# Kernel tuning notes

Hardware: AMD Instinct MI355X
Metric: run time of the kernel (lower is better)

## Reference

```python
import jax, jax.numpy as jnp
import numpy as np
import math

B, T, N_CTX, H = 4, 512, 2048, 1024
NUM_HEADS, NUM_INSTRUMENTS, MAX_BARS = 16, 16, 8
HEAD_DIM = H // NUM_HEADS


def setup_inputs() -> dict:
    key = jax.random.key(0)
    ks = jax.random.split(key, 16)
    s = 1.0 / math.sqrt(H)
    return {
        "query": jax.random.normal(ks[0], (B, T, H), jnp.float32),
        "context": jax.random.normal(ks[1], (B, N_CTX, H), jnp.float32),
        "instrument_ids": jax.random.randint(ks[2], (B, N_CTX), 0, NUM_INSTRUMENTS),
        "current_instrument_id": 3,
        "bar_offsets": jax.random.randint(ks[3], (B, N_CTX), 0, MAX_BARS),
        "Wq": jax.random.normal(ks[4], (H, H), jnp.float32) * s,
        "bq": jnp.zeros((H,), jnp.float32),
        "Wk": jax.random.normal(ks[5], (H, H), jnp.float32) * s,
        "bk": jnp.zeros((H,), jnp.float32),
        "Wv": jax.random.normal(ks[6], (H, H), jnp.float32) * s,
        "bv": jnp.zeros((H,), jnp.float32),
        "Wo": jax.random.normal(ks[7], (H, H), jnp.float32) * s,
        "bo": jnp.zeros((H,), jnp.float32),
        "inst_emb": jax.random.normal(ks[8], (NUM_INSTRUMENTS, H), jnp.float32),
        "bar_emb": jax.random.normal(ks[9], (MAX_BARS, H), jnp.float32),
    }


def reference(query, context, instrument_ids, current_instrument_id, bar_offsets,
              Wq, bq, Wk, bk, Wv, bv, Wo, bo, inst_emb, bar_emb):
    # current_instrument_id: python int -> broadcast to (B,)
    cur = jnp.full((B,), current_instrument_id, dtype=jnp.int64 if instrument_ids.dtype == jnp.int64 else jnp.int32)
    # add embeddings to query and context
    q = query + inst_emb[cur][:, None, :]                              # (B,T,H)
    ctx = context + inst_emb[instrument_ids] + bar_emb[jnp.clip(bar_offsets, 0, MAX_BARS - 1)]  # (B,N,H)
    # projections (torch Linear: x @ W.T + b)
    Q = (q @ Wq.T + bq).reshape(B, T, NUM_HEADS, HEAD_DIM).transpose(0, 2, 1, 3)      # (B,h,T,d)
    K = (ctx @ Wk.T + bk).reshape(B, N_CTX, NUM_HEADS, HEAD_DIM).transpose(0, 2, 1, 3)  # (B,h,N,d)
    V = (ctx @ Wv.T + bv).reshape(B, N_CTX, NUM_HEADS, HEAD_DIM).transpose(0, 2, 1, 3)  # (B,h,N,d)
    scores = jnp.einsum('bhtd,bhnd->bhtn', Q, K) / math.sqrt(HEAD_DIM)  # (B,h,T,N)
    # attend only to keys whose instrument differs from the current one
    keep = (instrument_ids != cur[:, None])[:, None, None, :]           # (B,1,1,N)
    scores = jnp.where(keep, scores, jnp.float32(-1e9))
    probs = jax.nn.softmax(scores, axis=-1)
    out = jnp.einsum('bhtn,bhnd->bhtd', probs, V).transpose(0, 2, 1, 3).reshape(B, T, H)
    return out @ Wo.T + bo
```

## Files before the change

kernel.cpp:

```cpp
#include <hip/hip_runtime.h>

#define H 1024
#define B_ 4
#define T_ 512
#define NCTX 2048
#define NH 16
#define HD 64

typedef __attribute__((ext_vector_type(8))) short bf16x8;
typedef __attribute__((ext_vector_type(4))) float f32x4;
typedef __attribute__((ext_vector_type(4))) short s16x4;

__device__ __forceinline__ ushort f2b(float f) {
  union { float f; unsigned u; } v; v.f = f;
  unsigned u = v.u;
  unsigned r = (u + 0x7FFFu + ((u >> 16) & 1u)) >> 16;
  return (ushort)r;
}

__device__ __forceinline__ unsigned cvt_pk_bf16(float lo, float hi) {
  unsigned r;
  asm("v_cvt_pk_bf16_f32 %0, %1, %2" : "=v"(r) : "v"(lo), "v"(hi));
  return r;
}

__device__ __forceinline__ void gld16(const void* g, void* l) {
  __builtin_amdgcn_global_load_lds((const __attribute__((address_space(1))) unsigned int*)g,
                                   (__attribute__((address_space(3))) unsigned int*)l, 16, 0, 0);
}


__global__ void prep_all(const float* __restrict__ query, const float* __restrict__ ctx,
                         const int* __restrict__ ids, const int* __restrict__ curp,
                         const int* __restrict__ bars,
                         const float* __restrict__ iemb, const float* __restrict__ bemb,
                         const float* __restrict__ Wq, const float* __restrict__ Wk,
                         const float* __restrict__ Wv, const float* __restrict__ Wo,
                         ushort* __restrict__ qin, ushort* __restrict__ ctxb,
                         ushort* __restrict__ Wqb, ushort* __restrict__ Wkb,
                         ushort* __restrict__ Wvb, ushort* __restrict__ Wob,
                         float* __restrict__ maskf) {
  int blk = blockIdx.x;
  if (blk < 8192) {
    int i = blk * 256 + threadIdx.x;
    int row = i >> 8;
    int c4 = i & 255;
    int id = ids[row];
    int bar = bars[row];
    bar = bar < 0 ? 0 : (bar > 7 ? 7 : bar);
    float4 v = ((const float4*)ctx)[i];
    float4 e = ((const float4*)(iemb + (size_t)id * H))[c4];
    float4 g = ((const float4*)(bemb + (size_t)bar * H))[c4];
    s16x4 o;
    o[0] = (short)f2b(v.x + e.x + g.x); o[1] = (short)f2b(v.y + e.y + g.y);
    o[2] = (short)f2b(v.z + e.z + g.z); o[3] = (short)f2b(v.w + e.w + g.w);
    ((s16x4*)ctxb)[i] = o;
  } else if (blk < 10240) {
    int cur = curp[0];
    int i = (blk - 8192) * 256 + threadIdx.x;
    int c4 = i & 255;
    float4 v = ((const float4*)query)[i];
    float4 e = ((const float4*)(iemb + (size_t)cur * H))[c4];
    s16x4 o;
    o[0] = (short)f2b(v.x + e.x); o[1] = (short)f2b(v.y + e.y);
    o[2] = (short)f2b(v.z + e.z); o[3] = (short)f2b(v.w + e.w);
    ((s16x4*)qin)[i] = o;
  } else if (blk < 14336) {
    int b2 = blk - 10240;
    int which = b2 >> 10;
    int i = (b2 & 1023) * 256 + threadIdx.x;
    const float* s = which == 0 ? Wq : which == 1 ? Wk : which == 2 ? Wv : Wo;
    ushort* d = which == 0 ? Wqb : which == 1 ? Wkb : which == 2 ? Wvb : Wob;
    float4 v = ((const float4*)s)[i];
    s16x4 o;
    o[0] = (short)f2b(v.x); o[1] = (short)f2b(v.y);
    o[2] = (short)f2b(v.z); o[3] = (short)f2b(v.w);
    ((s16x4*)d)[i] = o;
  } else {
    int cur = curp[0];
    int i = (blk - 14336) * 256 + threadIdx.x;
    maskf[i] = (ids[i] != cur) ? 0.f : -1e30f;
  }
}


__global__ __launch_bounds__(256) void proj_k(const ushort* __restrict__ Aq,
                                              const ushort* __restrict__ Actx,
                                              const ushort* __restrict__ WQ,
                                              const ushort* __restrict__ WK,
                                              const ushort* __restrict__ WV,
                                              const float* __restrict__ bQ,
                                              const float* __restrict__ bK,
                                              const float* __restrict__ bV,
                                              ushort* __restrict__ Qout,
                                              ushort* __restrict__ Kout,
                                              ushort* __restrict__ VTout) {
  const int id = blockIdx.x;
  const ushort* A;
  const ushort* W;
  const float* bias;
  int row0, col0, mode;
  ushort* Cout;
  if (id < 1024) {
    int xcd = id & 7, rest = id >> 3;
    int bx = rest & 15, by = (rest >> 4) * 8 + xcd;
    A = Actx; row0 = by * 128;
    if (bx < 8) { W = WK; bias = bK; col0 = bx * 128; mode = 0; Cout = Kout; }
    else        { W = WV; bias = bV; col0 = (bx - 8) * 128; mode = 1; Cout = VTout; }
  } else {
    int q = id - 1024;
    A = Aq; row0 = (q >> 3) * 128; col0 = (q & 7) * 128;
    W = WQ; bias = bQ; mode = 2; Cout = Qout;
  }

  __shared__ ushort As[2][128 * 32];
  __shared__ ushort Bs[2][128 * 32];
  const int tid = threadIdx.x;
  const int lane = tid & 63;
  const int wv = tid >> 6;
  const int wr = wv >> 1, wc = wv & 1;
  const int lo = lane & 15, hi = lane >> 4;

  f32x4 acc[4][4];
#pragma unroll
  for (int m = 0; m < 4; m++)
#pragma unroll
    for (int n = 0; n < 4; n++) acc[m][n] = (f32x4){0.f, 0.f, 0.f, 0.f};

#pragma unroll
  for (int c = 0; c < 2; c++) {
    int ia = wv * 128 + c * 64 + lane;
    int r = ia >> 2, s = ia & 3;
    int sg = s ^ (r & 3);
    gld16(A + (size_t)(row0 + r) * H + sg * 8, (char*)As[0] + (wv * 128 + c * 64) * 16);
    gld16(W + (size_t)(col0 + r) * H + sg * 8, (char*)Bs[0] + (wv * 128 + c * 64) * 16);
  }
  __syncthreads();

  int cur = 0;
  for (int kt = 0; kt < 32; kt++) {
    if (kt < 31) {
#pragma unroll
      for (int c = 0; c < 2; c++) {
        int ia = wv * 128 + c * 64 + lane;
        int r = ia >> 2, s = ia & 3;
        int sg = s ^ (r & 3);
        gld16(A + (size_t)(row0 + r) * H + (kt + 1) * 32 + sg * 8,
              (char*)As[cur ^ 1] + (wv * 128 + c * 64) * 16);
        gld16(W + (size_t)(col0 + r) * H + (kt + 1) * 32 + sg * 8,
              (char*)Bs[cur ^ 1] + (wv * 128 + c * 64) * 16);
      }
    }
    bf16x8 af[4], bfr[4];
#pragma unroll
    for (int m = 0; m < 4; m++) {
      int rr = wr * 64 + m * 16 + lo;
      af[m] = *(const bf16x8*)(As[cur] + rr * 32 + (hi ^ (rr & 3)) * 8);
    }
#pragma unroll
    for (int n = 0; n < 4; n++) {
      int rr = wc * 64 + n * 16 + lo;
      bfr[n] = *(const bf16x8*)(Bs[cur] + rr * 32 + (hi ^ (rr & 3)) * 8);
    }
#pragma unroll
    for (int m = 0; m < 4; m++)
#pragma unroll
      for (int n = 0; n < 4; n++)
        acc[m][n] = __builtin_amdgcn_mfma_f32_16x16x32_bf16(af[m], bfr[n], acc[m][n], 0, 0, 0);
    __syncthreads();
    cur ^= 1;
  }

#pragma unroll
  for (int m = 0; m < 4; m++) {
    int gr0 = row0 + wr * 64 + m * 16 + hi * 4;
#pragma unroll
    for (int n = 0; n < 4; n++) {
      int gc = col0 + wc * 64 + n * 16 + lo;
      float bv = bias[gc];
      if (mode == 0) {
#pragma unroll
        for (int r = 0; r < 4; r++)
          Cout[(size_t)(gr0 + r) * H + gc] = f2b(acc[m][n][r] + bv);
      } else if (mode == 1) {
        int bb = gr0 >> 11, n0 = gr0 & 2047;
        s16x4 o;
#pragma unroll
        for (int r = 0; r < 4; r++) o[r] = (short)f2b(acc[m][n][r] + bv);
        *(s16x4*)(Cout + (size_t)bb * (H * NCTX) + (size_t)gc * NCTX + n0) = o;
      } else {
#pragma unroll
        for (int r = 0; r < 4; r++)
          Cout[(size_t)(gr0 + r) * H + gc] = f2b((acc[m][n][r] + bv) * 0.125f);
      }
    }
  }
}


__global__ __launch_bounds__(256) void gemm_o(const ushort* __restrict__ A,
                                              const ushort* __restrict__ W,
                                              const float* __restrict__ bias,
                                              float* __restrict__ Cout) {
  __shared__ ushort As[2][128 * 32];
  __shared__ ushort Bs[2][128 * 32];
  const int tid = threadIdx.x;
  const int lane = tid & 63;
  const int wv = tid >> 6;
  const int wr = wv >> 1, wc = wv & 1;
  const int lo = lane & 15, hi = lane >> 4;
  const int row0 = blockIdx.y * 128, col0 = blockIdx.x * 128;

  f32x4 acc[4][4];
#pragma unroll
  for (int m = 0; m < 4; m++)
#pragma unroll
    for (int n = 0; n < 4; n++) acc[m][n] = (f32x4){0.f, 0.f, 0.f, 0.f};

#pragma unroll
  for (int c = 0; c < 2; c++) {
    int ia = wv * 128 + c * 64 + lane;
    int r = ia >> 2, s = ia & 3;
    int sg = s ^ (r & 3);
    gld16(A + (size_t)(row0 + r) * H + sg * 8, (char*)As[0] + (wv * 128 + c * 64) * 16);
    gld16(W + (size_t)(col0 + r) * H + sg * 8, (char*)Bs[0] + (wv * 128 + c * 64) * 16);
  }
  __syncthreads();

  int cur = 0;
  for (int kt = 0; kt < 32; kt++) {
    if (kt < 31) {
#pragma unroll
      for (int c = 0; c < 2; c++) {
        int ia = wv * 128 + c * 64 + lane;
        int r = ia >> 2, s = ia & 3;
        int sg = s ^ (r & 3);
        gld16(A + (size_t)(row0 + r) * H + (kt + 1) * 32 + sg * 8,
              (char*)As[cur ^ 1] + (wv * 128 + c * 64) * 16);
        gld16(W + (size_t)(col0 + r) * H + (kt + 1) * 32 + sg * 8,
              (char*)Bs[cur ^ 1] + (wv * 128 + c * 64) * 16);
      }
    }
    bf16x8 af[4], bfr[4];
#pragma unroll
    for (int m = 0; m < 4; m++) {
      int rr = wr * 64 + m * 16 + lo;
      af[m] = *(const bf16x8*)(As[cur] + rr * 32 + (hi ^ (rr & 3)) * 8);
    }
#pragma unroll
    for (int n = 0; n < 4; n++) {
      int rr = wc * 64 + n * 16 + lo;
      bfr[n] = *(const bf16x8*)(Bs[cur] + rr * 32 + (hi ^ (rr & 3)) * 8);
    }
#pragma unroll
    for (int m = 0; m < 4; m++)
#pragma unroll
      for (int n = 0; n < 4; n++)
        acc[m][n] = __builtin_amdgcn_mfma_f32_16x16x32_bf16(af[m], bfr[n], acc[m][n], 0, 0, 0);
    __syncthreads();
    cur ^= 1;
  }

#pragma unroll
  for (int m = 0; m < 4; m++) {
    int gr0 = row0 + wr * 64 + m * 16 + hi * 4;
#pragma unroll
    for (int n = 0; n < 4; n++) {
      int gc = col0 + wc * 64 + n * 16 + lo;
      float bv = bias[gc];
#pragma unroll
      for (int r = 0; r < 4; r++)
        Cout[(size_t)(gr0 + r) * H + gc] = acc[m][n][r] + bv;
    }
  }
}


#define NSPLIT 2
#define KVLEN (NCTX / NSPLIT)
#define NT_KV (KVLEN / 64)

__global__ __launch_bounds__(256) void attn_k(const ushort* __restrict__ Q,
                                              const ushort* __restrict__ K,
                                              const ushort* __restrict__ VT,
                                              const float* __restrict__ maskf,
                                              float* __restrict__ OPf,
                                              float* __restrict__ mlf) {
  __shared__ ushort Ks[64 * 64];
  __shared__ ushort Vs[64 * 64];
  __shared__ ushort Ps[4][16 * 64];
  const int blk = (blockIdx.x & 7) * 128 + (blockIdx.x >> 3);
  const int qt = blk & 7;
  const int h = (blk >> 3) & 15;
  const int b = (blk >> 7) & 3;
  const int p = blk >> 9;
  const int tid = threadIdx.x, lane = tid & 63, w = tid >> 6;
  const int lo = lane & 15, hi = lane >> 4;
  const int swz = (lo & 7) << 4;
  const int kvbase = p * KVLEN;

  const ushort* Qp = Q + ((size_t)(b * T_ + qt * 64 + w * 16 + lo)) * H + h * HD;
  bf16x8 qf0 = *(const bf16x8*)(Qp + hi * 8);
  bf16x8 qf1 = *(const bf16x8*)(Qp + 32 + hi * 8);

  f32x4 oacc[4];
#pragma unroll
  for (int d = 0; d < 4; d++) oacc[d] = (f32x4){0.f, 0.f, 0.f, 0.f};
  float mrow = -1e30f, lrow = 0.f;

  const float* maskb = maskf + b * NCTX;
  const ushort* Kbase = K + ((size_t)(b * NCTX)) * H + h * HD;
  const ushort* Vbase = VT + (size_t)b * (H * NCTX) + (size_t)(h * HD) * NCTX;

  const int sr = tid >> 3, ss = tid & 7;
  const int wb0 = (sr * 128 + ss * 16) ^ ((sr & 7) << 4);
  const int sr1 = (tid + 256) >> 3, ss1 = (tid + 256) & 7;
  const int wb1 = (sr1 * 128 + ss1 * 16) ^ ((sr1 & 7) << 4);

  bf16x8 kr0, kr1, vr0, vr1;
  kr0 = *(const bf16x8*)(Kbase + (size_t)(kvbase + sr) * H + ss * 8);
  vr0 = *(const bf16x8*)(Vbase + (size_t)sr * NCTX + kvbase + ss * 8);
  kr1 = *(const bf16x8*)(Kbase + (size_t)(kvbase + sr1) * H + ss1 * 8);
  vr1 = *(const bf16x8*)(Vbase + (size_t)sr1 * NCTX + kvbase + ss1 * 8);
  *(bf16x8*)((char*)Ks + wb0) = kr0;
  *(bf16x8*)((char*)Vs + wb0) = vr0;
  *(bf16x8*)((char*)Ks + wb1) = kr1;
  *(bf16x8*)((char*)Vs + wb1) = vr1;
  __syncthreads();

  for (int t = 0; t < NT_KV; t++) {
    int kvt = kvbase + t * 64;
    if (t < NT_KV - 1) {
      kr0 = *(const bf16x8*)(Kbase + (size_t)(kvt + 64 + sr) * H + ss * 8);
      vr0 = *(const bf16x8*)(Vbase + (size_t)sr * NCTX + kvt + 64 + ss * 8);
      kr1 = *(const bf16x8*)(Kbase + (size_t)(kvt + 64 + sr1) * H + ss1 * 8);
      vr1 = *(const bf16x8*)(Vbase + (size_t)sr1 * NCTX + kvt + 64 + ss1 * 8);
    }

    f32x4 sc[4];
    __builtin_amdgcn_s_setprio(1);
#pragma unroll
    for (int nt = 0; nt < 4; nt++) {
      bf16x8 kf0 = *(const bf16x8*)((char*)Ks + ((((nt * 16 + lo) * 128) + hi * 16) ^ swz));
      bf16x8 kf1 = *(const bf16x8*)((char*)Ks + ((((nt * 16 + lo) * 128) + 64 + hi * 16) ^ swz));
      f32x4 z = (f32x4){0.f, 0.f, 0.f, 0.f};
      z = __builtin_amdgcn_mfma_f32_16x16x32_bf16(kf0, qf0, z, 0, 0, 0);
      sc[nt] = __builtin_amdgcn_mfma_f32_16x16x32_bf16(kf1, qf1, z, 0, 0, 0);
    }
    __builtin_amdgcn_s_setprio(0);

    float pv[4][4];
#pragma unroll
    for (int nt = 0; nt < 4; nt++) {
      float4 mv = *(const float4*)(maskb + kvt + nt * 16 + hi * 4);
      pv[nt][0] = sc[nt][0] + mv.x;
      pv[nt][1] = sc[nt][1] + mv.y;
      pv[nt][2] = sc[nt][2] + mv.z;
      pv[nt][3] = sc[nt][3] + mv.w;
    }

    float m0 = fmaxf(fmaxf(pv[0][0], pv[0][1]), fmaxf(pv[0][2], pv[0][3]));
    float m1 = fmaxf(fmaxf(pv[1][0], pv[1][1]), fmaxf(pv[1][2], pv[1][3]));
    float m2 = fmaxf(fmaxf(pv[2][0], pv[2][1]), fmaxf(pv[2][2], pv[2][3]));
    float m3 = fmaxf(fmaxf(pv[3][0], pv[3][1]), fmaxf(pv[3][2], pv[3][3]));
    float x = fmaxf(fmaxf(m0, m1), fmaxf(m2, m3));
    x = fmaxf(x, __shfl_xor(x, 16));
    x = fmaxf(x, __shfl_xor(x, 32));
    bool defer = __all((x <= mrow + 8.0f) && (mrow > -1e29f));
    float mn, scal = 1.f;
    if (defer) {
      mn = mrow;
    } else {
      mn = fmaxf(mrow, x);
      scal = __expf(mrow - mn);
      mrow = mn;
    }
    float rsp[4];
#pragma unroll
    for (int nt = 0; nt < 4; nt++) {
      float e0 = __expf(pv[nt][0] - mn);
      float e1 = __expf(pv[nt][1] - mn);
      float e2 = __expf(pv[nt][2] - mn);
      float e3 = __expf(pv[nt][3] - mn);
      pv[nt][0] = e0; pv[nt][1] = e1; pv[nt][2] = e2; pv[nt][3] = e3;
      rsp[nt] = (e0 + e1) + (e2 + e3);
    }
    float rs = (rsp[0] + rsp[1]) + (rsp[2] + rsp[3]);
    rs += __shfl_xor(rs, 16);
    rs += __shfl_xor(rs, 32);
    if (defer) {
      lrow += rs;
    } else {
      lrow = lrow * scal + rs;
      float sq0 = __shfl(scal, hi * 4 + 0);
      float sq1 = __shfl(scal, hi * 4 + 1);
      float sq2 = __shfl(scal, hi * 4 + 2);
      float sq3 = __shfl(scal, hi * 4 + 3);
#pragma unroll
      for (int d = 0; d < 4; d++) {
        oacc[d][0] *= sq0; oacc[d][1] *= sq1; oacc[d][2] *= sq2; oacc[d][3] *= sq3;
      }
    }

#pragma unroll
    for (int nt = 0; nt < 4; nt++) {
      uint2 pw;
      pw.x = cvt_pk_bf16(pv[nt][0], pv[nt][1]);
      pw.y = cvt_pk_bf16(pv[nt][2], pv[nt][3]);
      *(uint2*)((char*)Ps[w] + ((lo * 128 + (nt * 16 + hi * 4) * 2) ^ swz)) = pw;
    }

    __builtin_amdgcn_s_setprio(1);
#pragma unroll
    for (int ks = 0; ks < 2; ks++) {
      bf16x8 pa = *(const bf16x8*)((char*)Ps[w] + ((lo * 128 + (ks * 64 + hi * 16)) ^ swz));
#pragma unroll
      for (int d = 0; d < 4; d++) {
        bf16x8 vf = *(const bf16x8*)((char*)Vs + (((d * 16 + lo) * 128 + ks * 64 + hi * 16) ^ swz));
        oacc[d] = __builtin_amdgcn_mfma_f32_16x16x32_bf16(pa, vf, oacc[d], 0, 0, 0);
      }
    }
    __builtin_amdgcn_s_setprio(0);

    if (t < NT_KV - 1) {
      __syncthreads();
      *(bf16x8*)((char*)Ks + wb0) = kr0;
      *(bf16x8*)((char*)Vs + wb0) = vr0;
      *(bf16x8*)((char*)Ks + wb1) = kr1;
      *(bf16x8*)((char*)Vs + wb1) = vr1;
      __syncthreads();
    }
  }

  int row0 = b * 512 + qt * 64 + w * 16 + hi * 4;
#pragma unroll
  for (int d = 0; d < 4; d++) {
#pragma unroll
    for (int r = 0; r < 4; r++)
      OPf[((size_t)p * 2048 + row0 + r) * 1024 + h * 64 + d * 16 + lo] = oacc[d][r];
  }
  if (hi == 0) {
    int qrow = b * 512 + qt * 64 + w * 16 + lo;
    mlf[(((size_t)p * 2048 + qrow) * 16 + h) * 2] = mrow;
    mlf[(((size_t)p * 2048 + qrow) * 16 + h) * 2 + 1] = lrow;
  }
}

__global__ void attn_combine(const float* __restrict__ OPf, const float* __restrict__ mlf,
                             ushort* __restrict__ O) {
  int idx = blockIdx.x * 256 + threadIdx.x;
  int btr = idx >> 8;
  int c4 = idx & 255;
  int h = c4 >> 4;
  float m0 = mlf[((size_t)btr * 16 + h) * 2];
  float l0 = mlf[((size_t)btr * 16 + h) * 2 + 1];
  float m1 = mlf[(((size_t)2048 + btr) * 16 + h) * 2];
  float l1 = mlf[(((size_t)2048 + btr) * 16 + h) * 2 + 1];
  float M = fmaxf(m0, m1);
  float a0 = __expf(m0 - M), a1 = __expf(m1 - M);
  float inv = 1.0f / (a0 * l0 + a1 * l1);
  float4 o0 = ((const float4*)OPf)[idx];
  float4 o1 = ((const float4*)OPf)[(size_t)524288 + idx];
  s16x4 r;
  r[0] = (short)f2b((a0 * o0.x + a1 * o1.x) * inv);
  r[1] = (short)f2b((a0 * o0.y + a1 * o1.y) * inv);
  r[2] = (short)f2b((a0 * o0.z + a1 * o1.z) * inv);
  r[3] = (short)f2b((a0 * o0.w + a1 * o1.w) * inv);
  ((s16x4*)O)[idx] = r;
}


extern "C" void kernel_launch(void* const* d_in, const int* in_sizes, int n_in,
                              void* d_out, int out_size, void* d_ws, size_t ws_size,
                              hipStream_t stream) {
  const float* query = (const float*)d_in[0];
  const float* context = (const float*)d_in[1];
  const int* ids = (const int*)d_in[2];
  const int* curp = (const int*)d_in[3];
  const int* bars = (const int*)d_in[4];
  const float* Wq = (const float*)d_in[5];
  const float* bq = (const float*)d_in[6];
  const float* Wk = (const float*)d_in[7];
  const float* bk = (const float*)d_in[8];
  const float* Wv = (const float*)d_in[9];
  const float* bv = (const float*)d_in[10];
  const float* Wo = (const float*)d_in[11];
  const float* bo = (const float*)d_in[12];
  const float* iemb = (const float*)d_in[13];
  const float* bemb = (const float*)d_in[14];
  float* out = (float*)d_out;

  ushort* ws = (ushort*)d_ws;
  ushort* Wqb = ws;
  ushort* Wkb = Wqb + (1u << 20);
  ushort* Wvb = Wkb + (1u << 20);
  ushort* Wob = Wvb + (1u << 20);
  ushort* qin = Wob + (1u << 20);
  ushort* ctxb = qin + (2u << 20);
  ushort* Qb = ctxb + (8u << 20);
  ushort* Kb = Qb + (2u << 20);
  ushort* VTb = Kb + (8u << 20);
  ushort* AOb = VTb + (8u << 20);

  float* OPf = (float*)ctxb;
  float* mlf = (float*)qin;
  float* maskf = out;

  prep_all<<<14368, 256, 0, stream>>>(query, context, ids, curp, bars, iemb, bemb,
                                      Wq, Wk, Wv, Wo, qin, ctxb, Wqb, Wkb, Wvb, Wob, maskf);

  proj_k<<<1152, 256, 0, stream>>>(qin, ctxb, Wqb, Wkb, Wvb, bq, bk, bv, Qb, Kb, VTb);

  attn_k<<<1024, 256, 0, stream>>>(Qb, Kb, VTb, maskf, OPf, mlf);
  attn_combine<<<2048, 256, 0, stream>>>(OPf, mlf, AOb);

  gemm_o<<<dim3(8, 16), 256, 0, stream>>>(AOb, Wob, bo, out);
}
```

Measured before the change: 160.8 us.

## Enlarge projection GEMM tile to 256x128 and drop LDS XOR swizzle

The QKV projection kernel now computes 256x128 output tiles per block (8x4 MFMA accumulators per wave) and launches half as many blocks, with an occupancy hint of 2 blocks per CU. The aim is to raise arithmetic intensity and cut redundant weight loads from global memory. Both the projection and output GEMMs also drop the XOR swizzle on LDS layout. That simplifies address math but risks LDS bank conflicts on the fragment reads, and the larger tile adds register pressure.

```diff
diff --git a/kernel.cpp b/kernel.cpp
--- a/kernel.cpp
+++ b/kernel.cpp
@@ -84,36 +84,37 @@
 }
 
 
-__global__ __launch_bounds__(256) void proj_k(const ushort* __restrict__ Aq,
-                                              const ushort* __restrict__ Actx,
-                                              const ushort* __restrict__ WQ,
-                                              const ushort* __restrict__ WK,
-                                              const ushort* __restrict__ WV,
-                                              const float* __restrict__ bQ,
-                                              const float* __restrict__ bK,
-                                              const float* __restrict__ bV,
-                                              ushort* __restrict__ Qout,
-                                              ushort* __restrict__ Kout,
-                                              ushort* __restrict__ VTout) {
+__global__ __launch_bounds__(256, 2) void proj_k(const ushort* __restrict__ Aq,
+                                                 const ushort* __restrict__ Actx,
+                                                 const ushort* __restrict__ WQ,
+                                                 const ushort* __restrict__ WK,
+                                                 const ushort* __restrict__ WV,
+                                                 const float* __restrict__ bQ,
+                                                 const float* __restrict__ bK,
+                                                 const float* __restrict__ bV,
+                                                 ushort* __restrict__ Qout,
+                                                 ushort* __restrict__ Kout,
+                                                 ushort* __restrict__ VTout) {
   const int id = blockIdx.x;
   const ushort* A;
   const ushort* W;
   const float* bias;
   int row0, col0, mode;
   ushort* Cout;
-  if (id < 1024) {
+  if (id < 512) {
     int xcd = id & 7, rest = id >> 3;
-    int bx = rest & 15, by = (rest >> 4) * 8 + xcd;
-    A = Actx; row0 = by * 128;
+    int bx = rest & 15;
+    int by = (rest >> 4) * 8 + xcd;
+    A = Actx; row0 = by * 256;
     if (bx < 8) { W = WK; bias = bK; col0 = bx * 128; mode = 0; Cout = Kout; }
     else        { W = WV; bias = bV; col0 = (bx - 8) * 128; mode = 1; Cout = VTout; }
   } else {
-    int q = id - 1024;
-    A = Aq; row0 = (q >> 3) * 128; col0 = (q & 7) * 128;
+    int q = id - 512;
+    A = Aq; row0 = (q >> 3) * 256; col0 = (q & 7) * 128;
     W = WQ; bias = bQ; mode = 2; Cout = Qout;
   }
 
-  __shared__ ushort As[2][128 * 32];
+  __shared__ ushort As[2][256 * 32];
   __shared__ ushort Bs[2][128 * 32];
   const int tid = threadIdx.x;
   const int lane = tid & 63;
@@ -121,49 +122,52 @@
   const int wr = wv >> 1, wc = wv & 1;
   const int lo = lane & 15, hi = lane >> 4;
 
-  f32x4 acc[4][4];
-#pragma unroll
-  for (int m = 0; m < 4; m++)
+  f32x4 acc[8][4];
+#pragma unroll
+  for (int m = 0; m < 8; m++)
 #pragma unroll
     for (int n = 0; n < 4; n++) acc[m][n] = (f32x4){0.f, 0.f, 0.f, 0.f};
 
 #pragma unroll
-  for (int c = 0; c < 2; c++) {
-    int ia = wv * 128 + c * 64 + lane;
+  for (int i = 0; i < 4; i++) {
+    int ia = tid + i * 256;
     int r = ia >> 2, s = ia & 3;
-    int sg = s ^ (r & 3);
-    gld16(A + (size_t)(row0 + r) * H + sg * 8, (char*)As[0] + (wv * 128 + c * 64) * 16);
-    gld16(W + (size_t)(col0 + r) * H + sg * 8, (char*)Bs[0] + (wv * 128 + c * 64) * 16);
+    gld16(A + (size_t)(row0 + r) * H + s * 8, (char*)As[0] + ia * 16);
+  }
+#pragma unroll
+  for (int i = 0; i < 2; i++) {
+    int ib = tid + i * 256;
+    int r = ib >> 2, s = ib & 3;
+    gld16(W + (size_t)(col0 + r) * H + s * 8, (char*)Bs[0] + ib * 16);
   }
   __syncthreads();
 
   int cur = 0;
   for (int kt = 0; kt < 32; kt++) {
     if (kt < 31) {
-#pragma unroll
-      for (int c = 0; c < 2; c++) {
-        int ia = wv * 128 + c * 64 + lane;
+      int ko = (kt + 1) * 32;
+#pragma unroll
+      for (int i = 0; i < 4; i++) {
+        int ia = tid + i * 256;
         int r = ia >> 2, s = ia & 3;
-        int sg = s ^ (r & 3);
-        gld16(A + (size_t)(row0 + r) * H + (kt + 1) * 32 + sg * 8,
-              (char*)As[cur ^ 1] + (wv * 128 + c * 64) * 16);
-        gld16(W + (size_t)(col0 + r) * H + (kt + 1) * 32 + sg * 8,
-              (char*)Bs[cur ^ 1] + (wv * 128 + c * 64) * 16);
+        gld16(A + (size_t)(row0 + r) * H + ko + s * 8, (char*)As[cur ^ 1] + ia * 16);
       }
-    }
-    bf16x8 af[4], bfr[4];
-#pragma unroll
-    for (int m = 0; m < 4; m++) {
-      int rr = wr * 64 + m * 16 + lo;
-      af[m] = *(const bf16x8*)(As[cur] + rr * 32 + (hi ^ (rr & 3)) * 8);
-    }
-#pragma unroll
-    for (int n = 0; n < 4; n++) {
-      int rr = wc * 64 + n * 16 + lo;
-      bfr[n] = *(const bf16x8*)(Bs[cur] + rr * 32 + (hi ^ (rr & 3)) * 8);
-    }
-#pragma unroll
-    for (int m = 0; m < 4; m++)
+#pragma unroll
+      for (int i = 0; i < 2; i++) {
+        int ib = tid + i * 256;
+        int r = ib >> 2, s = ib & 3;
+        gld16(W + (size_t)(col0 + r) * H + ko + s * 8, (char*)Bs[cur ^ 1] + ib * 16);
+      }
+    }
+    bf16x8 af[8], bfr[4];
+#pragma unroll
+    for (int m = 0; m < 8; m++)
+      af[m] = *(const bf16x8*)(As[cur] + (wr * 128 + m * 16 + lo) * 32 + hi * 8);
+#pragma unroll
+    for (int n = 0; n < 4; n++)
+      bfr[n] = *(const bf16x8*)(Bs[cur] + (wc * 64 + n * 16 + lo) * 32 + hi * 8);
+#pragma unroll
+    for (int m = 0; m < 8; m++)
 #pragma unroll
       for (int n = 0; n < 4; n++)
         acc[m][n] = __builtin_amdgcn_mfma_f32_16x16x32_bf16(af[m], bfr[n], acc[m][n], 0, 0, 0);
@@ -172,8 +176,8 @@
   }
 
 #pragma unroll
-  for (int m = 0; m < 4; m++) {
-    int gr0 = row0 + wr * 64 + m * 16 + hi * 4;
+  for (int m = 0; m < 8; m++) {
+    int gr0 = row0 + wr * 128 + m * 16 + hi * 4;
 #pragma unroll
     for (int n = 0; n < 4; n++) {
       int gc = col0 + wc * 64 + n * 16 + lo;
@@ -221,9 +225,8 @@
   for (int c = 0; c < 2; c++) {
     int ia = wv * 128 + c * 64 + lane;
     int r = ia >> 2, s = ia & 3;
-    int sg = s ^ (r & 3);
-    gld16(A + (size_t)(row0 + r) * H + sg * 8, (char*)As[0] + (wv * 128 + c * 64) * 16);
-    gld16(W + (size_t)(col0 + r) * H + sg * 8, (char*)Bs[0] + (wv * 128 + c * 64) * 16);
+    gld16(A + (size_t)(row0 + r) * H + s * 8, (char*)As[0] + (wv * 128 + c * 64) * 16);
+    gld16(W + (size_t)(col0 + r) * H + s * 8, (char*)Bs[0] + (wv * 128 + c * 64) * 16);
   }
   __syncthreads();
 
@@ -234,24 +237,17 @@
       for (int c = 0; c < 2; c++) {
         int ia = wv * 128 + c * 64 + lane;
         int r = ia >> 2, s = ia & 3;
-        int sg = s ^ (r & 3);
-        gld16(A + (size_t)(row0 + r) * H + (kt + 1) * 32 + sg * 8,
+        gld16(A + (size_t)(row0 + r) * H + (kt + 1) * 32 + s * 8,
               (char*)As[cur ^ 1] + (wv * 128 + c * 64) * 16);
-        gld16(W + (size_t)(col0 + r) * H + (kt + 1) * 32 + sg * 8,
+        gld16(W + (size_t)(col0 + r) * H + (kt + 1) * 32 + s * 8,
               (char*)Bs[cur ^ 1] + (wv * 128 + c * 64) * 16);
       }
     }
     bf16x8 af[4], bfr[4];
 #pragma unroll
-    for (int m = 0; m < 4; m++) {
-      int rr = wr * 64 + m * 16 + lo;
-      af[m] = *(const bf16x8*)(As[cur] + rr * 32 + (hi ^ (rr & 3)) * 8);
-    }
-#pragma unroll
-    for (int n = 0; n < 4; n++) {
-      int rr = wc * 64 + n * 16 + lo;
-      bfr[n] = *(const bf16x8*)(Bs[cur] + rr * 32 + (hi ^ (rr & 3)) * 8);
-    }
+    for (int m = 0; m < 4; m++) af[m] = *(const bf16x8*)(As[cur] + (wr * 64 + m * 16 + lo) * 32 + hi * 8);
+#pragma unroll
+    for (int n = 0; n < 4; n++) bfr[n] = *(const bf16x8*)(Bs[cur] + (wc * 64 + n * 16 + lo) * 32 + hi * 8);
 #pragma unroll
     for (int m = 0; m < 4; m++)
 #pragma unroll
@@ -509,7 +505,7 @@
   prep_all<<<14368, 256, 0, stream>>>(query, context, ids, curp, bars, iemb, bemb,
                                       Wq, Wk, Wv, Wo, qin, ctxb, Wqb, Wkb, Wvb, Wob, maskf);
 
-  proj_k<<<1152, 256, 0, stream>>>(qin, ctxb, Wqb, Wkb, Wvb, bq, bk, bv, Qb, Kb, VTb);
+  proj_k<<<576, 256, 0, stream>>>(qin, ctxb, Wqb, Wkb, Wvb, bq, bk, bv, Qb, Kb, VTb);
 
   attn_k<<<1024, 256, 0, stream>>>(Qb, Kb, VTb, maskf, OPf, mlf);
   attn_combine<<<2048, 256, 0, stream>>>(OPf, mlf, AOb);
```

Result: slower. 183.0 us (+13.8%).

## Triple-buffer QKV projection GEMM with vmcnt waits and drop LDS swizzle

Applied to the files above, without the earlier changes.

The fused QKV projection GEMM moves from a double-buffered LDS pipeline to a triple-buffered one. It prefetches two k-tiles ahead and uses explicit s_waitcnt vmcnt plus raw s_barrier in place of __syncthreads, so global loads stay in flight across iterations. Separately, both the QKV and output projection GEMMs drop the XOR swizzle on LDS rows in favour of a plain row-major layout. That simplifies addressing but risks LDS bank conflicts on the 16-byte fragment reads. The extra buffer raises LDS use per block, and the hand-counted vmcnt values must match the number of outstanding loads.

```diff
diff --git a/kernel.cpp b/kernel.cpp
--- a/kernel.cpp
+++ b/kernel.cpp
@@ -113,8 +113,8 @@
     W = WQ; bias = bQ; mode = 2; Cout = Qout;
   }
 
-  __shared__ ushort As[2][128 * 32];
-  __shared__ ushort Bs[2][128 * 32];
+  __shared__ ushort As[3][128 * 32];
+  __shared__ ushort Bs[3][128 * 32];
   const int tid = threadIdx.x;
   const int lane = tid & 63;
   const int wv = tid >> 6;
@@ -127,49 +127,48 @@
 #pragma unroll
     for (int n = 0; n < 4; n++) acc[m][n] = (f32x4){0.f, 0.f, 0.f, 0.f};
 
-#pragma unroll
-  for (int c = 0; c < 2; c++) {
-    int ia = wv * 128 + c * 64 + lane;
-    int r = ia >> 2, s = ia & 3;
-    int sg = s ^ (r & 3);
-    gld16(A + (size_t)(row0 + r) * H + sg * 8, (char*)As[0] + (wv * 128 + c * 64) * 16);
-    gld16(W + (size_t)(col0 + r) * H + sg * 8, (char*)Bs[0] + (wv * 128 + c * 64) * 16);
-  }
-  __syncthreads();
-
-  int cur = 0;
-  for (int kt = 0; kt < 32; kt++) {
-    if (kt < 31) {
-#pragma unroll
-      for (int c = 0; c < 2; c++) {
-        int ia = wv * 128 + c * 64 + lane;
-        int r = ia >> 2, s = ia & 3;
-        int sg = s ^ (r & 3);
-        gld16(A + (size_t)(row0 + r) * H + (kt + 1) * 32 + sg * 8,
-              (char*)As[cur ^ 1] + (wv * 128 + c * 64) * 16);
-        gld16(W + (size_t)(col0 + r) * H + (kt + 1) * 32 + sg * 8,
-              (char*)Bs[cur ^ 1] + (wv * 128 + c * 64) * 16);
-      }
-    }
+#define PSTAGE(KT, AB, BB)                                                              \
+  {                                                                                     \
+    int ko = (KT) * 32;                                                                 \
+    _Pragma("unroll") for (int c = 0; c < 2; c++) {                                     \
+      int ia = wv * 128 + c * 64 + lane;                                                \
+      int r = ia >> 2, s = ia & 3;                                                      \
+      gld16(A + (size_t)(row0 + r) * H + ko + s * 8, (char*)(AB) + (wv * 128 + c * 64) * 16); \
+      gld16(W + (size_t)(col0 + r) * H + ko + s * 8, (char*)(BB) + (wv * 128 + c * 64) * 16); \
+    }                                                                                   \
+  }
+
+  PSTAGE(0, As[0], Bs[0]);
+  PSTAGE(1, As[1], Bs[1]);
+  asm volatile("s_waitcnt vmcnt(4)" ::: "memory");
+  __builtin_amdgcn_s_barrier();
+
+  int bi = 0, si = 2;
+  for (int t = 0; t < 32; ++t) {
+    if (t + 2 < 32) PSTAGE(t + 2, As[si], Bs[si]);
+    const ushort* Ab = As[bi];
+    const ushort* Bb = Bs[bi];
     bf16x8 af[4], bfr[4];
 #pragma unroll
-    for (int m = 0; m < 4; m++) {
-      int rr = wr * 64 + m * 16 + lo;
-      af[m] = *(const bf16x8*)(As[cur] + rr * 32 + (hi ^ (rr & 3)) * 8);
-    }
-#pragma unroll
-    for (int n = 0; n < 4; n++) {
-      int rr = wc * 64 + n * 16 + lo;
-      bfr[n] = *(const bf16x8*)(Bs[cur] + rr * 32 + (hi ^ (rr & 3)) * 8);
-    }
+    for (int m = 0; m < 4; m++) af[m] = *(const bf16x8*)(Ab + (wr * 64 + m * 16 + lo) * 32 + hi * 8);
+#pragma unroll
+    for (int n = 0; n < 4; n++) bfr[n] = *(const bf16x8*)(Bb + (wc * 64 + n * 16 + lo) * 32 + hi * 8);
 #pragma unroll
     for (int m = 0; m < 4; m++)
 #pragma unroll
       for (int n = 0; n < 4; n++)
         acc[m][n] = __builtin_amdgcn_mfma_f32_16x16x32_bf16(af[m], bfr[n], acc[m][n], 0, 0, 0);
-    __syncthreads();
-    cur ^= 1;
-  }
+    if (t < 30) {
+      asm volatile("s_waitcnt vmcnt(4)" ::: "memory");
+      __builtin_amdgcn_s_barrier();
+    } else if (t == 30) {
+      asm volatile("s_waitcnt vmcnt(0)" ::: "memory");
+      __builtin_amdgcn_s_barrier();
+    }
+    bi = (bi == 2) ? 0 : bi + 1;
+    si = (si == 2) ? 0 : si + 1;
+  }
+#undef PSTAGE
 
 #pragma unroll
   for (int m = 0; m < 4; m++) {
@@ -221,9 +220,8 @@
   for (int c = 0; c < 2; c++) {
     int ia = wv * 128 + c * 64 + lane;
     int r = ia >> 2, s = ia & 3;
-    int sg = s ^ (r & 3);
-    gld16(A + (size_t)(row0 + r) * H + sg * 8, (char*)As[0] + (wv * 128 + c * 64) * 16);
-    gld16(W + (size_t)(col0 + r) * H + sg * 8, (char*)Bs[0] + (wv * 128 + c * 64) * 16);
+    gld16(A + (size_t)(row0 + r) * H + s * 8, (char*)As[0] + (wv * 128 + c * 64) * 16);
+    gld16(W + (size_t)(col0 + r) * H + s * 8, (char*)Bs[0] + (wv * 128 + c * 64) * 16);
   }
   __syncthreads();
 
@@ -234,24 +232,17 @@
       for (int c = 0; c < 2; c++) {
         int ia = wv * 128 + c * 64 + lane;
         int r = ia >> 2, s = ia & 3;
-        int sg = s ^ (r & 3);
-        gld16(A + (size_t)(row0 + r) * H + (kt + 1) * 32 + sg * 8,
+        gld16(A + (size_t)(row0 + r) * H + (kt + 1) * 32 + s * 8,
               (char*)As[cur ^ 1] + (wv * 128 + c * 64) * 16);
-        gld16(W + (size_t)(col0 + r) * H + (kt + 1) * 32 + sg * 8,
+        gld16(W + (size_t)(col0 + r) * H + (kt + 1) * 32 + s * 8,
               (char*)Bs[cur ^ 1] + (wv * 128 + c * 64) * 16);
       }
     }
     bf16x8 af[4], bfr[4];
 #pragma unroll
-    for (int m = 0; m < 4; m++) {
-      int rr = wr * 64 + m * 16 + lo;
-      af[m] = *(const bf16x8*)(As[cur] + rr * 32 + (hi ^ (rr & 3)) * 8);
-    }
-#pragma unroll
-    for (int n = 0; n < 4; n++) {
-      int rr = wc * 64 + n * 16 + lo;
-      bfr[n] = *(const bf16x8*)(Bs[cur] + rr * 32 + (hi ^ (rr & 3)) * 8);
-    }
+    for (int m = 0; m < 4; m++) af[m] = *(const bf16x8*)(As[cur] + (wr * 64 + m * 16 + lo) * 32 + hi * 8);
+#pragma unroll
+    for (int n = 0; n < 4; n++) bfr[n] = *(const bf16x8*)(Bs[cur] + (wc * 64 + n * 16 + lo) * 32 + hi * 8);
 #pragma unroll
     for (int m = 0; m < 4; m++)
 #pragma unroll
```

New measurement: 171.7 us. +6.8%, slower.
